# Optimization experiments

Hardware: AMD Instinct MI355X
Metric: run time of the kernel (lower is better)

Reference implementation:

```python
import jax, jax.numpy as jnp
import numpy as np

B, SEQ, D, INITIAL_D, T_DIFF = 256, 200, 256, 256, 1000


def _linear_params(key, fan_in, fan_out):
    k1, k2 = jax.random.split(key)
    lim = 1.0 / np.sqrt(fan_in)
    w = jax.random.uniform(k1, (fan_in, fan_out), minval=-lim, maxval=lim, dtype=jnp.float32)
    b = jax.random.uniform(k2, (fan_out,), minval=-lim, maxval=lim, dtype=jnp.float32)
    return w, b


def setup_inputs() -> dict:
    key = jax.random.key(0)
    ks = list(jax.random.split(key, 24))
    inp = {}
    inp["input_seqs"] = jax.random.normal(ks[0], (B, SEQ, INITIAL_D), dtype=jnp.float32)
    inp["masks"] = jnp.zeros((B, SEQ), dtype=jnp.int32)
    inp["lengths"] = jnp.full((B,), SEQ, dtype=jnp.int32)
    inp["seq_time_step"] = jax.random.uniform(ks[1], (B, SEQ), dtype=jnp.float32) * 360.0
    inp["code_masks"] = jnp.zeros((B, SEQ), dtype=jnp.int32)
    inp["diffusion_time_t"] = jax.random.randint(ks[2], (B,), 0, T_DIFF)
    inp["normal_noise"] = jax.random.normal(ks[3], (B, SEQ, D), dtype=jnp.float32)
    inp["predicted_noise"] = jax.random.normal(ks[4], (B, SEQ, D), dtype=jnp.float32) * 0.1
    inp["betas"] = jnp.linspace(1e-4, 0.02, T_DIFF, dtype=jnp.float32)
    names = [("emb2", INITIAL_D, D), ("Wall", D, 4 * D), ("Uall", D, 4 * D), ("Wd", D, D),
             ("time", 64, D), ("sel", 1, 64), ("whk", D, D), ("w1", 2 * D, 64),
             ("w2", 64, 2), ("out", D, 2)]
    for i, (nm, fi, fo) in enumerate(names):
        w, b = _linear_params(ks[5 + i], fi, fo)
        inp[nm + "_w"] = w
        inp[nm + "_b"] = b
    return inp


def reference(input_seqs, masks, lengths, seq_time_step, code_masks,
              diffusion_time_t, normal_noise, predicted_noise, betas,
              emb2_w, emb2_b, Wall_w, Wall_b, Uall_w, Uall_b, Wd_w, Wd_b,
              time_w, time_b, sel_w, sel_b, whk_w, whk_b,
              w1_w, w1_b, w2_w, w2_b, out_w, out_b):
    x = input_seqs @ emb2_w + emb2_b                      # [b,seq,d]  (initial_d != 0 path)
    b, seq, d = x.shape
    t = seq_time_step[..., None] / 180.0                  # [b,seq,1]
    tfeat = 1.0 - jnp.tanh(jnp.square(t @ sel_w + sel_b))  # [b,seq,64]
    time_feature = tfeat @ time_w + time_b                # [b,seq,d]

    def tlstm(xs_tmajor, tf_tmajor):
        # xs_tmajor, tf_tmajor: [seq, b, d] -> hidden states [b, seq, d]
        def step(carry, inp):
            h, c = carry
            xs, ts = inp
            c_s1 = jnp.tanh(c @ Wd_w + Wd_b)
            c_adj = c - c_s1 + c_s1 * ts                  # time-decayed cell
            gates = jax.nn.sigmoid(h @ Wall_w + Wall_b + xs @ Uall_w + Uall_b)
            f, i, o, ct = jnp.split(gates, 4, axis=-1)    # note: c_tmp uses sigmoid too
            c_new = f * c_adj + i * ct
            h_new = o * jnp.tanh(c_new)
            return (h_new, c_new), h_new
        zeros = jnp.zeros((xs_tmajor.shape[1], d), xs_tmajor.dtype)
        _, hs = jax.lax.scan(step, (zeros, zeros), (xs_tmajor, tf_tmajor))
        return hs.transpose(1, 0, 2)                      # [b,seq,d]

    tf_t = time_feature.transpose(1, 0, 2)
    outputs = tlstm(x.transpose(1, 0, 2), tf_t)

    # attention alignment (original always uses e_k = x[:, 0:1]) — fully vectorized over i>=1
    e_k = x[:, :1, :]                                     # [b,1,d]
    whk = outputs[:, :-1, :] @ whk_w + whk_b              # [b,seq-1,d]
    cat = jnp.concatenate([jnp.broadcast_to(e_k, whk.shape), whk], axis=-1)
    attn = jax.nn.softmax(jnp.tanh(cat @ w1_w + w1_b) @ w2_w + w2_b, axis=-1)  # [b,seq-1,2]
    aligned = jnp.concatenate([e_k, e_k * attn[..., 0:1] + whk * attn[..., 1:2]], axis=1)

    alpha = jnp.cumprod(1.0 - betas)[diffusion_time_t].reshape(-1, 1, 1)
    _noisy = aligned * jnp.sqrt(alpha) + normal_noise * jnp.sqrt(1.0 - alpha)  # UNet input (UNet output stubbed as predicted_noise)
    gen_x = aligned + (normal_noise - predicted_noise)
    gen_outputs = tlstm(gen_x.transpose(1, 0, 2), tf_t)

    out = jnp.max(outputs, axis=1) @ out_w + out_b        # max-pool over seq, then mlp
    gen_out = jnp.max(gen_outputs, axis=1) @ out_w + out_b
    return (out, gen_out, predicted_noise, normal_noise)
```

## Files before the change

kernel.cpp:

```cpp
#include <hip/hip_runtime.h>
#include <hip/hip_bf16.h>
#include <cstdint>

typedef __attribute__((ext_vector_type(8))) short short8;
typedef __attribute__((ext_vector_type(4))) float f32x4;
typedef unsigned short ushortT;

#define SEQ 200
#define NB  256

__device__ __forceinline__ float b2f(ushortT u){
    union { unsigned u; float f; } v; v.u = ((unsigned)u) << 16; return v.f;
}
__device__ __forceinline__ ushortT f2b(float f){
    union { float f; unsigned u; } v; v.f = f;
    unsigned r = v.u + 0x7FFFu + ((v.u >> 16) & 1u);
    return (ushortT)(r >> 16);
}
__device__ __forceinline__ float frcp(float x){
    float r; asm("v_rcp_f32 %0, %1" : "=v"(r) : "v"(x)); return r;
}
__device__ __forceinline__ float sigm(float x){ return frcp(1.0f + __expf(-x)); }
__device__ __forceinline__ float tanh_fast(float x){
    float ax = fabsf(x);
    float t = __expf(-2.0f * ax);
    float r = (1.0f - t) * frcp(1.0f + t);
    return copysignf(r, x);
}

__global__ void k_cvt(const float* __restrict__ in, ushortT* __restrict__ out){
    size_t i = ((size_t)blockIdx.x*256 + threadIdx.x)*4;
    float4 v = *(const float4*)(in + i);
    ushortT o[4] = { f2b(v.x), f2b(v.y), f2b(v.z), f2b(v.w) };
    *(int2*)(out + i) = *(int2*)o;
}

__global__ void k_swizzle(const float* __restrict__ src, int ncols,
                          ushortT* __restrict__ dst, int tile0){
    int Tl = blockIdx.x, q = blockIdx.y, l = threadIdx.x;
    int n  = Tl*16 + (l & 15);
    int kb = q*32 + (l >> 4)*8;
    short8 v;
    #pragma unroll
    for (int j = 0; j < 8; ++j) ((ushortT*)&v)[j] = f2b(src[(size_t)(kb + j)*ncols + n]);
    *(short8*)(dst + ((size_t)(tile0 + Tl)*8 + q)*512 + (size_t)l*8) = v;
}

__global__ void k_tft(const float* __restrict__ sts, const float* __restrict__ selw,
                      const float* __restrict__ selb, ushortT* __restrict__ tft){
    int l = threadIdx.x, g = blockIdx.x / SEQ, t = blockIdx.x % SEQ;
    int lm = l & 15, lq = l >> 4;
    float tv = sts[(size_t)(g*16 + lm)*SEQ + t] * (1.0f/180.0f);
    size_t base = (size_t)(g*SEQ + t)*1024 + (size_t)l*8;
    #pragma unroll
    for (int q = 0; q < 2; ++q){
        short8 v;
        #pragma unroll
        for (int j = 0; j < 8; ++j){
            int u = q*32 + lq*8 + j;
            float a = tv * selw[u] + selb[u];
            ((ushortT*)&v)[j] = f2b(1.0f - tanh_fast(a*a));
        }
        *(short8*)(tft + base + (size_t)q*512) = v;
    }
}

__global__ __launch_bounds__(512) void k_gemm256(const ushortT* A,
        const ushortT* __restrict__ Bswz, const float* __restrict__ bias, ushortT* out){
    __shared__ ushortT stage[16*256];
    int tid = threadIdx.x, w = tid >> 6, l = tid & 63, lm = l & 15, lq = l >> 4;
    size_t r0 = (size_t)blockIdx.x * 16;
    const f32x4 fz = {0.f,0.f,0.f,0.f};
    f32x4 acc[2] = {fz, fz};
    for (int q = 0; q < 8; ++q){
        short8 a = *(const short8*)(A + (r0 + lm)*256 + q*32 + lq*8);
        #pragma unroll
        for (int p = 0; p < 2; ++p){
            int T = 2*w + p;
            short8 b = *(const short8*)(Bswz + ((size_t)T*8 + q)*512 + (size_t)l*8);
            acc[p] = __builtin_amdgcn_mfma_f32_16x16x32_bf16(a, b, acc[p], 0, 0, 0);
        }
    }
    #pragma unroll
    for (int p = 0; p < 2; ++p){
        int n = (2*w + p)*16 + lm;
        float bs = bias[n];
        #pragma unroll
        for (int r = 0; r < 4; ++r)
            stage[(lq*4 + r)*256 + n] = f2b(acc[p][r] + bs);
    }
    __syncthreads();
    int row = tid >> 5, c8 = tid & 31;
    int4 v = *(const int4*)(stage + row*256 + c8*8);
    *(int4*)(out + (r0 + row)*256 + (size_t)c8*8) = v;
}

__global__ __launch_bounds__(512) void k_gemmgates(const ushortT* __restrict__ A,
        const ushortT* __restrict__ Bswz, const float* __restrict__ bW,
        const float* __restrict__ bU, ushortT* __restrict__ out){
    int tid = threadIdx.x, w = tid >> 6, l = tid & 63, lm = l & 15, lq = l >> 4;
    int g = blockIdx.x / SEQ, t = blockIdx.x % SEQ;
    const f32x4 fz = {0.f,0.f,0.f,0.f};
    f32x4 acc[8] = {fz,fz,fz,fz,fz,fz,fz,fz};
    const ushortT* Arow = A + ((size_t)(g*16 + lm)*SEQ + t)*256;
    for (int q = 0; q < 8; ++q){
        short8 a = *(const short8*)(Arow + q*32 + lq*8);
        #pragma unroll
        for (int gq = 0; gq < 4; ++gq)
        #pragma unroll
        for (int p = 0; p < 2; ++p){
            int T = gq*16 + 2*w + p;
            short8 b = *(const short8*)(Bswz + ((size_t)T*8 + q)*512 + (size_t)l*8);
            acc[gq*2+p] = __builtin_amdgcn_mfma_f32_16x16x32_bf16(a, b, acc[gq*2+p], 0, 0, 0);
        }
    }
    short8 ch[4];
    #pragma unroll
    for (int gq = 0; gq < 4; ++gq)
    #pragma unroll
    for (int p = 0; p < 2; ++p){
        int n = gq*256 + w*32 + p*16 + lm;
        float bs = bW[n] + bU[n];
        #pragma unroll
        for (int r = 0; r < 4; ++r)
            ((ushortT*)&ch[p*2 + (gq>>1)])[(gq&1)*4 + r] = f2b(acc[gq*2+p][r] + bs);
    }
    size_t base = (size_t)(g*SEQ + t)*16384 + (size_t)(w*64 + l)*32;
    #pragma unroll
    for (int ci = 0; ci < 4; ++ci) *(short8*)(out + base + ci*8) = ch[ci];
}

__global__ void k_zeroflags(unsigned* __restrict__ f){
    f[blockIdx.x*256 + threadIdx.x] = 0;
}

#define HB (16*264)
__global__ __launch_bounds__(512, 2) void k_scan(const ushortT* __restrict__ xg,
        const ushortT* __restrict__ tftg, const ushortT* __restrict__ Wswz,
        const ushortT* __restrict__ twswz, const float* __restrict__ wdb_g,
        const float* __restrict__ timeb, ushortT* __restrict__ hs,
        float* __restrict__ maxh, int write_hs,
        ushortT* __restrict__ xbuf, unsigned* __restrict__ flags, unsigned fb){
    extern __shared__ ushortT smem[];
    ushortT* wlds = smem + 4*HB;
    int tid = threadIdx.x, w = tid >> 6, l = tid & 63, lm = l & 15, lq = l >> 4;
    int blk = blockIdx.x;
    int h = blk >> 4, g = blk & 15;
    int pblk = (1 - h)*16 + g;
    int cw = h*8 + w;
    int col = cw*16 + lm;
    int l8 = l*8;
    float wdb = wdb_g[col];
    float tb  = timeb[col];
    short8 twf[2];
    #pragma unroll
    for (int q2 = 0; q2 < 2; ++q2)
        twf[q2] = *(const short8*)(twswz + ((size_t)cw*8 + q2)*512 + l8);
    short8 wg0[8], wg1[8], wg2[8], wdreg[8];
    #pragma unroll
    for (int q = 0; q < 8; ++q){
        wg0[q]   = *(const short8*)(Wswz + ((size_t)( 0 + cw)*8 + q)*512 + l8);
        wg1[q]   = *(const short8*)(Wswz + ((size_t)(16 + cw)*8 + q)*512 + l8);
        wg2[q]   = *(const short8*)(Wswz + ((size_t)(32 + cw)*8 + q)*512 + l8);
        wdreg[q] = *(const short8*)(Wswz + ((size_t)(64 + cw)*8 + q)*512 + l8);
    }
    float c[4], hm[4];
    #pragma unroll
    for (int i = 0; i < 4; ++i){ c[i] = 0.0f; hm[i] = -2.0f; }
    for (int i = tid; i < HB; i += 512){ smem[HB + i] = 0; smem[3*HB + i] = 0; }
    {
        const int4* wsrc = (const int4*)(Wswz + (size_t)(48 + h*8)*4096);
        int4* wdst = (int4*)wlds;
        for (int i = tid; i < 4096; i += 512) wdst[i] = wsrc[i];
    }
    __syncthreads();

    const ushortT* xg_g  = xg   + (size_t)g*SEQ*16384 + ((size_t)(cw>>1)*64 + l)*32 + (cw&1)*16;
    const ushortT* tft_g = tftg + (size_t)g*SEQ*1024  + (size_t)l8;
    const ushortT* wl    = wlds + (size_t)w*4096 + l8;
    const f32x4 fz = {0.f,0.f,0.f,0.f};

    for (int t = 0; t < SEQ; ++t){
        int pb = t & 1, ab = 1 - pb;
        const ushortT* hb = smem + (size_t)ab*HB;
        const ushortT* cb = smem + 2*HB + (size_t)ab*HB;
        short8 xA  = *(const short8*)(xg_g + (size_t)t*16384);
        short8 xB  = *(const short8*)(xg_g + (size_t)t*16384 + 8);
        short8 aT0 = *(const short8*)(tft_g + (size_t)t*1024);
        short8 aT1 = *(const short8*)(tft_g + (size_t)t*1024 + 512);

        f32x4 acc[5];
        #pragma unroll
        for (int i = 0; i < 5; ++i) acc[i] = fz;
        #pragma unroll
        for (int q = 0; q < 8; ++q){
            short8 a  = *(const short8*)(hb + lm*264 + q*32 + lq*8);
            short8 ca = *(const short8*)(cb + lm*264 + q*32 + lq*8);
            short8 b3 = *(const short8*)(wl + q*512);
            acc[0] = __builtin_amdgcn_mfma_f32_16x16x32_bf16(a,  wg0[q],   acc[0], 0, 0, 0);
            acc[1] = __builtin_amdgcn_mfma_f32_16x16x32_bf16(a,  wg1[q],   acc[1], 0, 0, 0);
            acc[2] = __builtin_amdgcn_mfma_f32_16x16x32_bf16(a,  wg2[q],   acc[2], 0, 0, 0);
            acc[3] = __builtin_amdgcn_mfma_f32_16x16x32_bf16(a,  b3,       acc[3], 0, 0, 0);
            acc[4] = __builtin_amdgcn_mfma_f32_16x16x32_bf16(ca, wdreg[q], acc[4], 0, 0, 0);
        }
        f32x4 acc_ts = fz;
        acc_ts = __builtin_amdgcn_mfma_f32_16x16x32_bf16(aT0, twf[0], acc_ts, 0, 0, 0);
        acc_ts = __builtin_amdgcn_mfma_f32_16x16x32_bf16(aT1, twf[1], acc_ts, 0, 0, 0);

        ushortT* hbw = smem + (size_t)pb*HB;
        ushortT* cbw = smem + 2*HB + (size_t)pb*HB;
        #pragma unroll
        for (int r = 0; r < 4; ++r){
            float F   = acc[0][r] + b2f(((const ushortT*)&xA)[r]);
            float I   = acc[1][r] + b2f(((const ushortT*)&xA)[4+r]);
            float O   = acc[2][r] + b2f(((const ushortT*)&xB)[r]);
            float CT  = acc[3][r] + b2f(((const ushortT*)&xB)[4+r]);
            float cwd = acc[4][r] + wdb;
            float ts  = acc_ts[r] + tb;
            float cc  = c[r];
            float cs1 = tanh_fast(cwd);
            float cadj = cc - cs1 + cs1*ts;
            float cn  = sigm(F)*cadj + sigm(I)*sigm(CT);
            float hv  = sigm(O)*tanh_fast(cn);
            c[r]  = cn;
            hm[r] = fmaxf(hm[r], hv);
            hbw[(lq*4 + r)*264 + col] = f2b(hv);
            cbw[(lq*4 + r)*264 + col] = f2b(cn);
        }
        __syncthreads();
        if (write_hs && tid < 256){
            int row = tid >> 4, c16 = tid & 15;
            int4 v = *(const int4*)(hbw + row*264 + h*128 + c16*8);
            *(int4*)(hs + ((size_t)(g*16 + row)*SEQ + t)*256 + h*128 + c16*8) = v;
        }
        if (t < SEQ-1){
            {
                int part = tid >> 8, i = tid & 255, row = i >> 4, c16 = i & 15;
                const ushortT* src = (part ? cbw : hbw) + row*264 + h*128 + c16*8;
                union { int4 v; unsigned long long u[2]; } u; u.v = *(const int4*)src;
                unsigned long long* dst = (unsigned long long*)(xbuf +
                    ((((size_t)blk*2 + (t & 1))*2 + part)*16 + row)*128 + c16*8);
                __hip_atomic_store(dst+0, u.u[0], __ATOMIC_RELAXED, __HIP_MEMORY_SCOPE_AGENT);
                __hip_atomic_store(dst+1, u.u[1], __ATOMIC_RELAXED, __HIP_MEMORY_SCOPE_AGENT);
            }
            __syncthreads();
            if (tid == 0){
                unsigned want = fb + (unsigned)t + 1u;
                __hip_atomic_store(&flags[(size_t)blk*64], want,
                                   __ATOMIC_RELEASE, __HIP_MEMORY_SCOPE_AGENT);
                for (int it = 0; it < 20000000; ++it){
                    if (__hip_atomic_load(&flags[(size_t)pblk*64],
                            __ATOMIC_ACQUIRE, __HIP_MEMORY_SCOPE_AGENT) >= want) break;
                    __builtin_amdgcn_s_sleep(2);
                }
            }
            __syncthreads();
            {
                int part = tid >> 8, i = tid & 255, row = i >> 4, c16 = i & 15;
                const unsigned long long* src = (const unsigned long long*)(xbuf +
                    ((((size_t)pblk*2 + (t & 1))*2 + part)*16 + row)*128 + c16*8);
                union { int4 v; unsigned long long u[2]; } u;
                u.u[0] = __hip_atomic_load(src+0, __ATOMIC_RELAXED, __HIP_MEMORY_SCOPE_AGENT);
                u.u[1] = __hip_atomic_load(src+1, __ATOMIC_RELAXED, __HIP_MEMORY_SCOPE_AGENT);
                ushortT* dst = (part ? cbw : hbw) + row*264 + (1-h)*128 + c16*8;
                *(int4*)dst = u.v;
            }
            __syncthreads();
        }
    }
    #pragma unroll
    for (int r = 0; r < 4; ++r)
        maxh[(size_t)(g*16 + lq*4 + r)*256 + col] = hm[r];
}

__global__ void k_ekcopy(const ushortT* __restrict__ x, ushortT* __restrict__ ek){
    int b = blockIdx.x, l = threadIdx.x;
    ((int2*)(ek + (size_t)b*256))[l] = ((const int2*)(x + (size_t)b*SEQ*256))[l];
}

__global__ void k_ekw(const ushortT* __restrict__ ek, const float* __restrict__ w1w,
                      const float* __restrict__ w1b, float* __restrict__ ekw){
    int b = blockIdx.x, l = threadIdx.x;
    float acc = w1b[l];
    const ushortT* e = ek + (size_t)b*256;
    for (int d = 0; d < 256; ++d)
        acc += b2f(e[d]) * w1w[(size_t)d*64 + l];
    ekw[b*64 + l] = acc;
}

__global__ __launch_bounds__(512) void k_attn(const ushortT* __restrict__ ekbuf,
        const ushortT* __restrict__ whk, const float* __restrict__ ekw,
        const float* __restrict__ w1w, const float* __restrict__ w2w,
        const float* __restrict__ w2b, const float* __restrict__ nn,
        const float* __restrict__ pn, ushortT* __restrict__ genx){
    int w = threadIdx.x >> 6, l = threadIdx.x & 63;
    int wid = blockIdx.x*8 + w;
    int b = wid / SEQ, sp = wid % SEQ;
    const ushortT* ek = ekbuf + (size_t)b*256;
    const ushortT* wr = whk + ((size_t)b*SEQ + (sp > 0 ? sp-1 : 0))*256;
    size_t orow = ((size_t)b*SEQ + sp)*256;
    float a0, a1;
    if (sp == 0){ a0 = 1.0f; a1 = 0.0f; }
    else {
        float acc = ekw[b*64 + l];
        for (int d = 0; d < 256; ++d)
            acc += b2f(wr[d]) * w1w[(size_t)(256 + d)*64 + l];
        float u  = tanh_fast(acc);
        float p0 = u * w2w[l*2 + 0];
        float p1 = u * w2w[l*2 + 1];
        #pragma unroll
        for (int off = 32; off >= 1; off >>= 1){
            p0 += __shfl_xor(p0, off, 64);
            p1 += __shfl_xor(p1, off, 64);
        }
        float v0 = p0 + w2b[0], v1 = p1 + w2b[1];
        a0 = sigm(v0 - v1); a1 = 1.0f - a0;
    }
    #pragma unroll
    for (int i = 0; i < 4; ++i){
        int d = i*64 + l;
        float al = b2f(ek[d])*a0 + b2f(wr[d])*a1;
        float gv = al + nn[orow + d] - pn[orow + d];
        genx[orow + d] = f2b(gv);
    }
}

__global__ void k_final(const float* __restrict__ mh1, const float* __restrict__ mh2,
                        const float* __restrict__ ow, const float* __restrict__ ob,
                        float* __restrict__ outp){
    int th = threadIdx.x;
    const float* mh = blockIdx.x ? mh2 : mh1;
    int b = th >> 1, cc = th & 1;
    float acc = ob[cc];
    for (int d = 0; d < 256; ++d)
        acc += mh[b*256 + d] * ow[d*2 + cc];
    outp[blockIdx.x*512 + th] = acc;
}

extern "C" void kernel_launch(void* const* d_in, const int* in_sizes, int n_in,
                              void* d_out, int out_size, void* d_ws, size_t ws_size,
                              hipStream_t stream) {
    const float* input_seqs = (const float*)d_in[0];
    const float* seq_time   = (const float*)d_in[3];
    const float* nn     = (const float*)d_in[6];
    const float* pn     = (const float*)d_in[7];
    const float* emb2_w = (const float*)d_in[9];
    const float* emb2_b = (const float*)d_in[10];
    const float* Wall_w = (const float*)d_in[11];
    const float* Wall_b = (const float*)d_in[12];
    const float* Uall_w = (const float*)d_in[13];
    const float* Uall_b = (const float*)d_in[14];
    const float* Wd_w   = (const float*)d_in[15];
    const float* Wd_b   = (const float*)d_in[16];
    const float* time_w = (const float*)d_in[17];
    const float* time_b = (const float*)d_in[18];
    const float* sel_w  = (const float*)d_in[19];
    const float* sel_b  = (const float*)d_in[20];
    const float* whk_w  = (const float*)d_in[21];
    const float* whk_b  = (const float*)d_in[22];
    const float* w1_w   = (const float*)d_in[23];
    const float* w1_b   = (const float*)d_in[24];
    const float* w2_w   = (const float*)d_in[25];
    const float* w2_b   = (const float*)d_in[26];
    const float* out_w  = (const float*)d_in[27];
    const float* out_b  = (const float*)d_in[28];

    const size_t NSZ = (size_t)in_sizes[6];

    static bool attr_done = false;
    if (!attr_done){
        hipFuncSetAttribute((const void*)k_scan,
                            hipFuncAttributeMaxDynamicSharedMemorySize, 160*1024);
        attr_done = true;
    }
    const size_t SCAN_LDS = (size_t)(4*HB + 8*4096) * sizeof(ushortT);

    char* wsb = (char*)d_ws;
    size_t off = 0;
    auto alloc = [&](size_t bytes){ void* p = wsb + off; off += (bytes + 255) & ~(size_t)255; return p; };
    ushortT* Wswz  = (ushortT*)alloc(80u*8*512*2);
    ushortT* Uswz  = (ushortT*)alloc(64u*8*512*2);
    ushortT* Eswz  = (ushortT*)alloc(16u*8*512*2);
    ushortT* Hswz  = (ushortT*)alloc(16u*8*512*2);
    ushortT* TWswz = (ushortT*)alloc(16u*8*512*2);
    ushortT* TFT   = (ushortT*)alloc((size_t)16*SEQ*1024*2);
    ushortT* X     = (ushortT*)alloc((size_t)NB*SEQ*256*2);
    ushortT* XG    = (ushortT*)alloc((size_t)16*SEQ*16384*2);
    ushortT* HS    = (ushortT*)alloc((size_t)NB*SEQ*256*2);
    ushortT* EK    = (ushortT*)alloc((size_t)NB*256*2);
    float*  MAXH1  = (float*)alloc((size_t)NB*256*4);
    float*  MAXH2  = (float*)alloc((size_t)NB*256*4);
    float*  EKW    = (float*)alloc((size_t)NB*64*4);
    ushortT* XBUF  = (ushortT*)alloc((size_t)32*2*2*16*128*2);
    unsigned* FLAGS= (unsigned*)alloc((size_t)32*64*4);

    float* outp = (float*)d_out;
    hipMemcpyAsync(outp + 1024,       pn, NSZ*4, hipMemcpyDeviceToDevice, stream);
    hipMemcpyAsync(outp + 1024 + NSZ, nn, NSZ*4, hipMemcpyDeviceToDevice, stream);

    k_zeroflags<<<8, 256, 0, stream>>>(FLAGS);
    k_swizzle<<<dim3(64,8), 64, 0, stream>>>(Wall_w, 1024, Wswz, 0);
    k_swizzle<<<dim3(16,8), 64, 0, stream>>>(Wd_w,    256, Wswz, 64);
    k_swizzle<<<dim3(64,8), 64, 0, stream>>>(Uall_w, 1024, Uswz, 0);
    k_swizzle<<<dim3(16,8), 64, 0, stream>>>(emb2_w,  256, Eswz, 0);
    k_swizzle<<<dim3(16,8), 64, 0, stream>>>(whk_w,   256, Hswz, 0);
    k_swizzle<<<dim3(16,2), 64, 0, stream>>>(time_w,  256, TWswz, 0);

    k_tft<<<3200, 64, 0, stream>>>(seq_time, sel_w, sel_b, TFT);
    k_cvt<<<12800, 256, 0, stream>>>(input_seqs, HS);
    k_gemm256<<<3200, 512, 0, stream>>>(HS, Eswz, emb2_b, X);
    k_ekcopy<<<256, 64, 0, stream>>>(X, EK);
    k_ekw<<<256, 64, 0, stream>>>(EK, w1_w, w1_b, EKW);
    k_gemmgates<<<3200, 512, 0, stream>>>(X, Uswz, Wall_b, Uall_b, XG);
    k_scan<<<32, 512, SCAN_LDS, stream>>>(XG, TFT, Wswz, TWswz, Wd_b, time_b, HS, MAXH1, 1,
                                          XBUF, FLAGS, 0u);
    k_gemm256<<<3200, 512, 0, stream>>>(HS, Hswz, whk_b, HS);
    k_attn<<<6400, 512, 0, stream>>>(EK, HS, EKW, w1_w, w2_w, w2_b, nn, pn, X);
    k_gemmgates<<<3200, 512, 0, stream>>>(X, Uswz, Wall_b, Uall_b, XG);
    k_scan<<<32, 512, SCAN_LDS, stream>>>(XG, TFT, Wswz, TWswz, Wd_b, time_b, HS, MAXH2, 0,
                                          XBUF, FLAGS, (unsigned)SEQ);
    k_final<<<2, 512, 0, stream>>>(MAXH1, MAXH2, out_w, out_b, outp);
}
```

Before: 2.194 ms.

## Overlap partner-half exchange with local-half MFMAs in recurrent scan

```diff
diff --git a/kernel.cpp b/kernel.cpp
--- a/kernel.cpp
+++ b/kernel.cpp
@@ -3,6 +3,7 @@
 #include <cstdint>
 
 typedef __attribute__((ext_vector_type(8))) short short8;
+typedef __attribute__((ext_vector_type(4))) short short4v;
 typedef __attribute__((ext_vector_type(4))) float f32x4;
 typedef unsigned short ushortT;
 
@@ -150,6 +151,8 @@
     int cw = h*8 + w;
     int col = cw*16 + lm;
     int l8 = l*8;
+    int qlo = h*4;
+    int qro = (1 - h)*4;
     float wdb = wdb_g[col];
     float tb  = timeb[col];
     short8 twf[2];
@@ -182,8 +185,8 @@
 
     for (int t = 0; t < SEQ; ++t){
         int pb = t & 1, ab = 1 - pb;
-        const ushortT* hb = smem + (size_t)ab*HB;
-        const ushortT* cb = smem + 2*HB + (size_t)ab*HB;
+        ushortT* hb = smem + (size_t)ab*HB;
+        ushortT* cb = smem + 2*HB + (size_t)ab*HB;
         short8 xA  = *(const short8*)(xg_g + (size_t)t*16384);
         short8 xB  = *(const short8*)(xg_g + (size_t)t*16384 + 8);
         short8 aT0 = *(const short8*)(tft_g + (size_t)t*1024);
@@ -193,7 +196,8 @@
         #pragma unroll
         for (int i = 0; i < 5; ++i) acc[i] = fz;
         #pragma unroll
-        for (int q = 0; q < 8; ++q){
+        for (int qi = 0; qi < 4; ++qi){
+            int q = qlo + qi;
             short8 a  = *(const short8*)(hb + lm*264 + q*32 + lq*8);
             short8 ca = *(const short8*)(cb + lm*264 + q*32 + lq*8);
             short8 b3 = *(const short8*)(wl + q*512);
@@ -206,6 +210,42 @@
         f32x4 acc_ts = fz;
         acc_ts = __builtin_amdgcn_mfma_f32_16x16x32_bf16(aT0, twf[0], acc_ts, 0, 0, 0);
         acc_ts = __builtin_amdgcn_mfma_f32_16x16x32_bf16(aT1, twf[1], acc_ts, 0, 0, 0);
+
+        if (t > 0){
+            unsigned want = fb + (unsigned)t;
+            for (int it = 0; it < 20000000; ++it){
+                if (__hip_atomic_load(&flags[(size_t)pblk*64],
+                        __ATOMIC_ACQUIRE, __HIP_MEMORY_SCOPE_AGENT) >= want) break;
+                __builtin_amdgcn_s_sleep(1);
+            }
+            int row = tid >> 5, seg = tid & 31;
+            const unsigned long long* src = (const unsigned long long*)(xbuf +
+                ((size_t)(pblk*2 + ab)*16 + row)*256 + seg*8);
+            unsigned long long u0 = __hip_atomic_load(src+0, __ATOMIC_RELAXED, __HIP_MEMORY_SCOPE_AGENT);
+            unsigned long long u1 = __hip_atomic_load(src+1, __ATOMIC_RELAXED, __HIP_MEMORY_SCOPE_AGENT);
+            ushortT* hdst = hb + row*264 + (1-h)*128 + seg*4;
+            ushortT* cdst = cb + row*264 + (1-h)*128 + seg*4;
+            short4v hv4, cv4;
+            hv4[0] = (short)(ushortT)(u0);       cv4[0] = (short)(ushortT)(u0 >> 16);
+            hv4[1] = (short)(ushortT)(u0 >> 32); cv4[1] = (short)(ushortT)(u0 >> 48);
+            hv4[2] = (short)(ushortT)(u1);       cv4[2] = (short)(ushortT)(u1 >> 16);
+            hv4[3] = (short)(ushortT)(u1 >> 32); cv4[3] = (short)(ushortT)(u1 >> 48);
+            *(short4v*)hdst = hv4;
+            *(short4v*)cdst = cv4;
+            __syncthreads();
+        }
+        #pragma unroll
+        for (int qi = 0; qi < 4; ++qi){
+            int q = qro + qi;
+            short8 a  = *(const short8*)(hb + lm*264 + q*32 + lq*8);
+            short8 ca = *(const short8*)(cb + lm*264 + q*32 + lq*8);
+            short8 b3 = *(const short8*)(wl + q*512);
+            acc[0] = __builtin_amdgcn_mfma_f32_16x16x32_bf16(a,  wg0[q],   acc[0], 0, 0, 0);
+            acc[1] = __builtin_amdgcn_mfma_f32_16x16x32_bf16(a,  wg1[q],   acc[1], 0, 0, 0);
+            acc[2] = __builtin_amdgcn_mfma_f32_16x16x32_bf16(a,  wg2[q],   acc[2], 0, 0, 0);
+            acc[3] = __builtin_amdgcn_mfma_f32_16x16x32_bf16(a,  b3,       acc[3], 0, 0, 0);
+            acc[4] = __builtin_amdgcn_mfma_f32_16x16x32_bf16(ca, wdreg[q], acc[4], 0, 0, 0);
+        }
 
         ushortT* hbw = smem + (size_t)pb*HB;
         ushortT* cbw = smem + 2*HB + (size_t)pb*HB;
@@ -224,48 +264,24 @@
             float hv  = sigm(O)*tanh_fast(cn);
             c[r]  = cn;
             hm[r] = fmaxf(hm[r], hv);
-            hbw[(lq*4 + r)*264 + col] = f2b(hv);
-            cbw[(lq*4 + r)*264 + col] = f2b(cn);
+            ushortT hbf = f2b(hv), cbf = f2b(cn);
+            hbw[(lq*4 + r)*264 + col] = hbf;
+            cbw[(lq*4 + r)*264 + col] = cbf;
+            if (t < SEQ-1){
+                unsigned hc = (unsigned)hbf | ((unsigned)cbf << 16);
+                unsigned* xd = (unsigned*)(xbuf +
+                    ((size_t)(blk*2 + pb)*16 + (lq*4 + r))*256 + (size_t)(w*16 + lm)*2);
+                __hip_atomic_store(xd, hc, __ATOMIC_RELAXED, __HIP_MEMORY_SCOPE_AGENT);
+            }
         }
         __syncthreads();
+        if (t < SEQ-1 && tid == 0)
+            __hip_atomic_store(&flags[(size_t)blk*64], fb + (unsigned)t + 1u,
+                               __ATOMIC_RELEASE, __HIP_MEMORY_SCOPE_AGENT);
         if (write_hs && tid < 256){
             int row = tid >> 4, c16 = tid & 15;
             int4 v = *(const int4*)(hbw + row*264 + h*128 + c16*8);
             *(int4*)(hs + ((size_t)(g*16 + row)*SEQ + t)*256 + h*128 + c16*8) = v;
-        }
-        if (t < SEQ-1){
-            {
-                int part = tid >> 8, i = tid & 255, row = i >> 4, c16 = i & 15;
-                const ushortT* src = (part ? cbw : hbw) + row*264 + h*128 + c16*8;
-                union { int4 v; unsigned long long u[2]; } u; u.v = *(const int4*)src;
-                unsigned long long* dst = (unsigned long long*)(xbuf +
-                    ((((size_t)blk*2 + (t & 1))*2 + part)*16 + row)*128 + c16*8);
-                __hip_atomic_store(dst+0, u.u[0], __ATOMIC_RELAXED, __HIP_MEMORY_SCOPE_AGENT);
-                __hip_atomic_store(dst+1, u.u[1], __ATOMIC_RELAXED, __HIP_MEMORY_SCOPE_AGENT);
-            }
-            __syncthreads();
-            if (tid == 0){
-                unsigned want = fb + (unsigned)t + 1u;
-                __hip_atomic_store(&flags[(size_t)blk*64], want,
-                                   __ATOMIC_RELEASE, __HIP_MEMORY_SCOPE_AGENT);
-                for (int it = 0; it < 20000000; ++it){
-                    if (__hip_atomic_load(&flags[(size_t)pblk*64],
-                            __ATOMIC_ACQUIRE, __HIP_MEMORY_SCOPE_AGENT) >= want) break;
-                    __builtin_amdgcn_s_sleep(2);
-                }
-            }
-            __syncthreads();
-            {
-                int part = tid >> 8, i = tid & 255, row = i >> 4, c16 = i & 15;
-                const unsigned long long* src = (const unsigned long long*)(xbuf +
-                    ((((size_t)pblk*2 + (t & 1))*2 + part)*16 + row)*128 + c16*8);
-                union { int4 v; unsigned long long u[2]; } u;
-                u.u[0] = __hip_atomic_load(src+0, __ATOMIC_RELAXED, __HIP_MEMORY_SCOPE_AGENT);
-                u.u[1] = __hip_atomic_load(src+1, __ATOMIC_RELAXED, __HIP_MEMORY_SCOPE_AGENT);
-                ushortT* dst = (part ? cbw : hbw) + row*264 + (1-h)*128 + c16*8;
-                *(int4*)dst = u.v;
-            }
-            __syncthreads();
         }
     }
     #pragma unroll
@@ -391,7 +407,7 @@
     float*  MAXH1  = (float*)alloc((size_t)NB*256*4);
     float*  MAXH2  = (float*)alloc((size_t)NB*256*4);
     float*  EKW    = (float*)alloc((size_t)NB*64*4);
-    ushortT* XBUF  = (ushortT*)alloc((size_t)32*2*2*16*128*2);
+    ushortT* XBUF  = (ushortT*)alloc((size_t)32*2*16*256*2);
     unsigned* FLAGS= (unsigned*)alloc((size_t)32*64*4);
 
     float* outp = (float*)d_out;
```

New measurement: 3.655 ms. +66.6%, slower.

## Compute attention w1 projection with MFMA GEMM and overlap hs stores with flag wait

Applied to the files above, without the earlier changes.

```diff
diff --git a/kernel.cpp b/kernel.cpp
--- a/kernel.cpp
+++ b/kernel.cpp
@@ -93,6 +93,22 @@
     int row = tid >> 5, c8 = tid & 31;
     int4 v = *(const int4*)(stage + row*256 + c8*8);
     *(int4*)(out + (r0 + row)*256 + (size_t)c8*8) = v;
+}
+
+__global__ __launch_bounds__(256) void k_gemm64(const ushortT* __restrict__ A,
+        const ushortT* __restrict__ Bswz, float* __restrict__ out){
+    int tid = threadIdx.x, w = tid >> 6, l = tid & 63, lm = l & 15, lq = l >> 4;
+    size_t r0 = (size_t)blockIdx.x * 16;
+    const f32x4 fz = {0.f,0.f,0.f,0.f};
+    f32x4 acc = fz;
+    for (int q = 0; q < 8; ++q){
+        short8 a = *(const short8*)(A + (r0 + lm)*256 + q*32 + lq*8);
+        short8 b = *(const short8*)(Bswz + ((size_t)w*8 + q)*512 + (size_t)l*8);
+        acc = __builtin_amdgcn_mfma_f32_16x16x32_bf16(a, b, acc, 0, 0, 0);
+    }
+    #pragma unroll
+    for (int r = 0; r < 4; ++r)
+        out[(r0 + lq*4 + r)*64 + w*16 + lm] = acc[r];
 }
 
 __global__ __launch_bounds__(512) void k_gemmgates(const ushortT* __restrict__ A,
@@ -228,44 +244,51 @@
             cbw[(lq*4 + r)*264 + col] = f2b(cn);
         }
         __syncthreads();
-        if (write_hs && tid < 256){
-            int row = tid >> 4, c16 = tid & 15;
-            int4 v = *(const int4*)(hbw + row*264 + h*128 + c16*8);
-            *(int4*)(hs + ((size_t)(g*16 + row)*SEQ + t)*256 + h*128 + c16*8) = v;
-        }
         if (t < SEQ-1){
             {
                 int part = tid >> 8, i = tid & 255, row = i >> 4, c16 = i & 15;
                 const ushortT* src = (part ? cbw : hbw) + row*264 + h*128 + c16*8;
-                union { int4 v; unsigned long long u[2]; } u; u.v = *(const int4*)src;
+                union { int4 v; unsigned long long uu[2]; } u; u.v = *(const int4*)src;
                 unsigned long long* dst = (unsigned long long*)(xbuf +
-                    ((((size_t)blk*2 + (t & 1))*2 + part)*16 + row)*128 + c16*8);
-                __hip_atomic_store(dst+0, u.u[0], __ATOMIC_RELAXED, __HIP_MEMORY_SCOPE_AGENT);
-                __hip_atomic_store(dst+1, u.u[1], __ATOMIC_RELAXED, __HIP_MEMORY_SCOPE_AGENT);
+                    ((((size_t)blk*2 + pb)*2 + part)*16 + row)*128 + c16*8);
+                __hip_atomic_store(dst+0, u.uu[0], __ATOMIC_RELAXED, __HIP_MEMORY_SCOPE_AGENT);
+                __hip_atomic_store(dst+1, u.uu[1], __ATOMIC_RELAXED, __HIP_MEMORY_SCOPE_AGENT);
             }
             __syncthreads();
             if (tid == 0){
+                __hip_atomic_store(&flags[(size_t)blk*64], fb + (unsigned)t + 1u,
+                                   __ATOMIC_RELEASE, __HIP_MEMORY_SCOPE_AGENT);
                 unsigned want = fb + (unsigned)t + 1u;
-                __hip_atomic_store(&flags[(size_t)blk*64], want,
-                                   __ATOMIC_RELEASE, __HIP_MEMORY_SCOPE_AGENT);
                 for (int it = 0; it < 20000000; ++it){
                     if (__hip_atomic_load(&flags[(size_t)pblk*64],
                             __ATOMIC_ACQUIRE, __HIP_MEMORY_SCOPE_AGENT) >= want) break;
                     __builtin_amdgcn_s_sleep(2);
                 }
             }
+            if (write_hs && tid >= 256){
+                int i = tid - 256, row = i >> 4, c16 = i & 15;
+                int4 v = *(const int4*)(hbw + row*264 + h*128 + c16*8);
+                *(int4*)(hs + ((size_t)(g*16 + row)*SEQ + t)*256 + h*128 + c16*8) = v;
+            }
             __syncthreads();
             {
                 int part = tid >> 8, i = tid & 255, row = i >> 4, c16 = i & 15;
                 const unsigned long long* src = (const unsigned long long*)(xbuf +
-                    ((((size_t)pblk*2 + (t & 1))*2 + part)*16 + row)*128 + c16*8);
-                union { int4 v; unsigned long long u[2]; } u;
-                u.u[0] = __hip_atomic_load(src+0, __ATOMIC_RELAXED, __HIP_MEMORY_SCOPE_AGENT);
-                u.u[1] = __hip_atomic_load(src+1, __ATOMIC_RELAXED, __HIP_MEMORY_SCOPE_AGENT);
+                    ((((size_t)pblk*2 + pb)*2 + part)*16 + row)*128 + c16*8);
+                unsigned long long u0 = __hip_atomic_load(src+0, __ATOMIC_RELAXED, __HIP_MEMORY_SCOPE_AGENT);
+                unsigned long long u1 = __hip_atomic_load(src+1, __ATOMIC_RELAXED, __HIP_MEMORY_SCOPE_AGENT);
                 ushortT* dst = (part ? cbw : hbw) + row*264 + (1-h)*128 + c16*8;
+                union { int4 v; unsigned long long uu[2]; } u;
+                u.uu[0] = u0; u.uu[1] = u1;
                 *(int4*)dst = u.v;
             }
             __syncthreads();
+        } else {
+            if (write_hs && tid < 256){
+                int row = tid >> 4, c16 = tid & 15;
+                int4 v = *(const int4*)(hbw + row*264 + h*128 + c16*8);
+                *(int4*)(hs + ((size_t)(g*16 + row)*SEQ + t)*256 + h*128 + c16*8) = v;
+            }
         }
     }
     #pragma unroll
@@ -290,7 +313,7 @@
 
 __global__ __launch_bounds__(512) void k_attn(const ushortT* __restrict__ ekbuf,
         const ushortT* __restrict__ whk, const float* __restrict__ ekw,
-        const float* __restrict__ w1w, const float* __restrict__ w2w,
+        const float* __restrict__ w1p, const float* __restrict__ w2w,
         const float* __restrict__ w2b, const float* __restrict__ nn,
         const float* __restrict__ pn, ushortT* __restrict__ genx){
     int w = threadIdx.x >> 6, l = threadIdx.x & 63;
@@ -302,9 +325,7 @@
     float a0, a1;
     if (sp == 0){ a0 = 1.0f; a1 = 0.0f; }
     else {
-        float acc = ekw[b*64 + l];
-        for (int d = 0; d < 256; ++d)
-            acc += b2f(wr[d]) * w1w[(size_t)(256 + d)*64 + l];
+        float acc = ekw[b*64 + l] + w1p[((size_t)b*SEQ + sp-1)*64 + l];
         float u  = tanh_fast(acc);
         float p0 = u * w2w[l*2 + 0];
         float p1 = u * w2w[l*2 + 1];
@@ -383,6 +404,7 @@
     ushortT* Eswz  = (ushortT*)alloc(16u*8*512*2);
     ushortT* Hswz  = (ushortT*)alloc(16u*8*512*2);
     ushortT* TWswz = (ushortT*)alloc(16u*8*512*2);
+    ushortT* W1swz = (ushortT*)alloc(4u*8*512*2);
     ushortT* TFT   = (ushortT*)alloc((size_t)16*SEQ*1024*2);
     ushortT* X     = (ushortT*)alloc((size_t)NB*SEQ*256*2);
     ushortT* XG    = (ushortT*)alloc((size_t)16*SEQ*16384*2);
@@ -391,6 +413,7 @@
     float*  MAXH1  = (float*)alloc((size_t)NB*256*4);
     float*  MAXH2  = (float*)alloc((size_t)NB*256*4);
     float*  EKW    = (float*)alloc((size_t)NB*64*4);
+    float*  W1P    = (float*)alloc((size_t)NB*SEQ*64*4);
     ushortT* XBUF  = (ushortT*)alloc((size_t)32*2*2*16*128*2);
     unsigned* FLAGS= (unsigned*)alloc((size_t)32*64*4);
 
@@ -405,6 +428,7 @@
     k_swizzle<<<dim3(16,8), 64, 0, stream>>>(emb2_w,  256, Eswz, 0);
     k_swizzle<<<dim3(16,8), 64, 0, stream>>>(whk_w,   256, Hswz, 0);
     k_swizzle<<<dim3(16,2), 64, 0, stream>>>(time_w,  256, TWswz, 0);
+    k_swizzle<<<dim3(4,8),  64, 0, stream>>>(w1_w + 256*64, 64, W1swz, 0);
 
     k_tft<<<3200, 64, 0, stream>>>(seq_time, sel_w, sel_b, TFT);
     k_cvt<<<12800, 256, 0, stream>>>(input_seqs, HS);
@@ -415,7 +439,8 @@
     k_scan<<<32, 512, SCAN_LDS, stream>>>(XG, TFT, Wswz, TWswz, Wd_b, time_b, HS, MAXH1, 1,
                                           XBUF, FLAGS, 0u);
     k_gemm256<<<3200, 512, 0, stream>>>(HS, Hswz, whk_b, HS);
-    k_attn<<<6400, 512, 0, stream>>>(EK, HS, EKW, w1_w, w2_w, w2_b, nn, pn, X);
+    k_gemm64<<<3200, 256, 0, stream>>>(HS, W1swz, W1P);
+    k_attn<<<6400, 512, 0, stream>>>(EK, HS, EKW, W1P, w2_w, w2_b, nn, pn, X);
     k_gemmgates<<<3200, 512, 0, stream>>>(X, Uswz, Wall_b, Uall_b, XG);
     k_scan<<<32, 512, SCAN_LDS, stream>>>(XG, TFT, Wswz, TWswz, Wd_b, time_b, HS, MAXH2, 0,
                                           XBUF, FLAGS, (unsigned)SEQ);
```

Measured after the change: 2.116 ms. 3.5% less time.
